# Kernel optimization log

Hardware: AMD Instinct MI355X
Metric: run time of the kernel (lower is better)

Reference implementation:

```python
import jax, jax.numpy as jnp
import numpy as np

D_IN = 2048
D_OUT = 2048
BOUND = 1.0


def setup_inputs() -> dict:
    key = jax.random.key(0)
    kx, kw = jax.random.split(key)
    x = jax.random.normal(kx, (4, 2048, D_IN), dtype=jnp.float32)
    W_raw = 0.02 * jax.random.normal(kw, (D_OUT, D_IN), dtype=jnp.float32)
    return {"x": x, "W_raw": W_raw}


def reference(x, W_raw):
    # sigma = ||W||_2 (largest singular value), exact via SVD
    sigma = jnp.linalg.svd(W_raw, full_matrices=False, compute_uv=False)[0]
    scale = jnp.maximum(sigma / BOUND, 1.0)  # clamp(sigma/bound, min=1)
    Wn = W_raw / scale                        # [d_out, d_in]
    return jnp.einsum('bsi,oi->bso', x, Wn)   # x @ Wn.T
```

## Files before the change

kernel.cpp:

```cpp
#include <hip/hip_runtime.h>
#include <stdint.h>

typedef short bf16x8 __attribute__((ext_vector_type(8)));
typedef float f32x4 __attribute__((ext_vector_type(4)));

__device__ __forceinline__ unsigned short f2bf(float f) {
  union { float f; unsigned int u; } v; v.f = f;
  unsigned int u = v.u;
  return (unsigned short)((u + 0x7FFFu + ((u >> 16) & 1u)) >> 16);
}
__device__ __forceinline__ float bf2f(unsigned short u) {
  union { unsigned int u; float f; } v; v.u = ((unsigned int)u) << 16;
  return v.f;
}
__device__ __forceinline__ void async16(const void* g, void* l) {
  __builtin_amdgcn_global_load_lds(
      (const __attribute__((address_space(1))) unsigned int*)g,
      (__attribute__((address_space(3))) unsigned int*)l, 16, 0, 0);
}

__global__ __launch_bounds__(256) void cast_f32_bf16(
    const float* __restrict__ in, unsigned short* __restrict__ out, int n8) {
  int i = blockIdx.x * 256 + threadIdx.x;
  if (i >= n8) return;
  const float4* p = (const float4*)in;
  float4 a = p[2 * (size_t)i], b = p[2 * (size_t)i + 1];
  union { bf16x8 v; unsigned short s[8]; } o;
  o.s[0] = f2bf(a.x); o.s[1] = f2bf(a.y); o.s[2] = f2bf(a.z); o.s[3] = f2bf(a.w);
  o.s[4] = f2bf(b.x); o.s[5] = f2bf(b.y); o.s[6] = f2bf(b.z); o.s[7] = f2bf(b.w);
  *(bf16x8*)(out + 8 * (size_t)i) = o.v;
}

__device__ __forceinline__ void stage16k(const unsigned short* __restrict__ g0,
                                         int ldK, unsigned short* lds, int tid) {
#pragma unroll
  for (int q = 0; q < 2; ++q) {
    int idx = q * 512 + tid;
    int r = idx >> 3;
    int jj = (idx & 7) ^ (r & 7);
    async16(g0 + (size_t)r * ldK + jj * 8,
            lds + ((size_t)(q * 512 + (tid & ~63))) * 8);
  }
}

template <int OMODE>
__global__ __launch_bounds__(512, 2) void gemm256(
    const unsigned short* __restrict__ A, const unsigned short* __restrict__ B,
    void* __restrict__ Cv, int M, int N, int lda, int K,
    int nTn, int mT, const float* __restrict__ scale_ptr) {
  __shared__ __align__(16) unsigned short AsBuf[3][256 * 64];
  __shared__ __align__(16) unsigned short BsBuf[2][256 * 64];
  const int tid = threadIdx.x;
  const int w = tid >> 6, lane = tid & 63;
  int bid = blockIdx.x;
  const int mb = bid % mT; bid /= mT;
  const int nb = bid % nTn; const int ks = bid / nTn;
  const int m0 = mb * 256, n0 = nb * 256;
  const int wr = w >> 2, wc = w & 3;
  const int R = K >> 7;

  const unsigned short* Ab = A + (size_t)m0 * lda + (size_t)ks * K;
  const unsigned short* Bb = B + (size_t)n0 * lda + (size_t)ks * K;

  unsigned short *a0 = AsBuf[0], *a1 = AsBuf[1], *a2 = AsBuf[2];
  unsigned short *b0 = BsBuf[0], *b1 = BsBuf[1];

  stage16k(Ab,                          lda, a0,            tid);
  stage16k(Ab + (size_t)128 * lda,      lda, a0 + 128 * 64, tid);
  stage16k(Bb,                          lda, b0,            tid);
  stage16k(Bb + (size_t)128 * lda,      lda, b0 + 128 * 64, tid);
  stage16k(Ab + 64,                     lda, a1,            tid);
  stage16k(Ab + 64 + (size_t)128 * lda, lda, a1 + 128 * 64, tid);
  stage16k(Bb + 64,                     lda, b1,            tid);
  stage16k(Bb + 64 + (size_t)128 * lda, lda, b1 + 128 * 64, tid);
  asm volatile("s_waitcnt vmcnt(8)" ::: "memory");
  __builtin_amdgcn_s_barrier();
  asm volatile("" ::: "memory");

  const int fr = lane & 15;
  const int bc0 = ((lane >> 4) << 4) ^ ((fr & 7) << 4);
  const int bc1 = bc0 ^ 64;

  f32x4 acc[8][4] = {};

  for (int r = 0; r < R; ++r) {
    const bool st = (r + 1 < R);
    bf16x8 bg[4][2];
#pragma unroll
    for (int ph = 0; ph < 8; ++ph) {
      const int d = ph >> 2, q = ph & 3;
      const char* cA = (const char*)(d == 0 ? a0 : a1);
      const char* cB = (const char*)(d == 0 ? b0 : b1);
      if (q == 0) {
#pragma unroll
        for (int nf = 0; nf < 4; ++nf) {
          int rb = (wc * 64 + nf * 16 + fr) * 128;
          bg[nf][0] = *(const bf16x8*)(cB + rb + bc0);
          bg[nf][1] = *(const bf16x8*)(cB + rb + bc1);
        }
      }
      bf16x8 af[2][2];
#pragma unroll
      for (int m2 = 0; m2 < 2; ++m2) {
        int rb = (wr * 128 + q * 32 + m2 * 16 + fr) * 128;
        af[m2][0] = *(const bf16x8*)(cA + rb + bc0);
        af[m2][1] = *(const bf16x8*)(cA + rb + bc1);
      }
      if (st) switch (ph) {
        case 0: stage16k(Ab + (size_t)(2 * r + 2) * 64, lda, a2, tid); break;
        case 1: stage16k(Ab + (size_t)(2 * r + 2) * 64 + (size_t)128 * lda, lda,
                         a2 + 128 * 64, tid); break;
        case 2: stage16k(Bb + (size_t)(2 * r + 2) * 64, lda, b0, tid); break;
        case 3: stage16k(Bb + (size_t)(2 * r + 2) * 64 + (size_t)128 * lda, lda,
                         b0 + 128 * 64, tid); break;
        case 4: stage16k(Ab + (size_t)(2 * r + 3) * 64, lda, a0, tid); break;
        case 5: stage16k(Ab + (size_t)(2 * r + 3) * 64 + (size_t)128 * lda, lda,
                         a0 + 128 * 64, tid); break;
        case 6: stage16k(Bb + (size_t)(2 * r + 3) * 64, lda, b1, tid); break;
        case 7: stage16k(Bb + (size_t)(2 * r + 3) * 64 + (size_t)128 * lda, lda,
                         b1 + 128 * 64, tid); break;
      }
      asm volatile("" ::: "memory");
      __builtin_amdgcn_s_barrier();
      asm volatile("" ::: "memory");
      __builtin_amdgcn_s_setprio(1);
#pragma unroll
      for (int m2 = 0; m2 < 2; ++m2)
#pragma unroll
        for (int nf = 0; nf < 4; ++nf)
#pragma unroll
          for (int kh = 0; kh < 2; ++kh)
            acc[q * 2 + m2][nf] = __builtin_amdgcn_mfma_f32_16x16x32_bf16(
                af[m2][kh], bg[nf][kh], acc[q * 2 + m2][nf], 0, 0, 0);
      __builtin_amdgcn_s_setprio(0);
      asm volatile("" ::: "memory");
      if (ph == 3) {
        if (st) asm volatile("s_waitcnt vmcnt(8)" ::: "memory");
        else    asm volatile("s_waitcnt vmcnt(0)" ::: "memory");
      } else if (ph == 7) {
        if (st) asm volatile("s_waitcnt vmcnt(8)" ::: "memory");
      }
      __builtin_amdgcn_s_barrier();
      asm volatile("" ::: "memory");
    }
    unsigned short* t = a2; a2 = a1; a1 = a0; a0 = t;
  }

  float sc = 1.0f;
  if (OMODE == 1) sc = *scale_ptr;
  size_t base = (OMODE == 2) ? (size_t)ks * ((size_t)M * N) : 0;
  const int rr0 = m0 + wr * 128 + ((lane >> 4) << 2);
  const int cc0 = n0 + wc * 64 + fr;
#pragma unroll
  for (int mf = 0; mf < 8; ++mf)
#pragma unroll
    for (int nf = 0; nf < 4; ++nf)
#pragma unroll
      for (int tt = 0; tt < 4; ++tt) {
        size_t idx = base + (size_t)(rr0 + mf * 16 + tt) * N + (cc0 + nf * 16);
        if (OMODE == 2) ((unsigned short*)Cv)[idx] = f2bf(acc[mf][nf][tt]);
        else            ((float*)Cv)[idx] = acc[mf][nf][tt] * sc;
      }
}

__global__ __launch_bounds__(256) void reduce_planes_init(
    const unsigned short* __restrict__ P, unsigned short* __restrict__ out,
    int n8, int np, size_t plane, float* __restrict__ t0,
    float* __restrict__ czero) {
  int i = blockIdx.x * 256 + threadIdx.x;
  if (blockIdx.x < 8) {
    int j = blockIdx.x * 256 + threadIdx.x;
    unsigned int h = (unsigned int)j * 2654435761u;
    h ^= h >> 16; h *= 2246822519u; h ^= h >> 13;
    t0[j] = (float)(h & 0xFFFFu) * (1.0f / 65536.0f) - 0.5f;
    if (j == 0) czero[0] = 0.0f;
  }
  if (i >= n8) return;
  float s[8] = {0.f, 0.f, 0.f, 0.f, 0.f, 0.f, 0.f, 0.f};
  for (int p = 0; p < np; ++p) {
    bf16x8 v = *(const bf16x8*)(P + (size_t)p * plane + (size_t)i * 8);
#pragma unroll
    for (int j = 0; j < 8; ++j) s[j] += bf2f((unsigned short)v[j]);
  }
  union { bf16x8 v; unsigned short u[8]; } o;
#pragma unroll
  for (int j = 0; j < 8; ++j) o.u[j] = f2bf(s[j]);
  *(bf16x8*)(out + (size_t)i * 8) = o.v;
}

__global__ __launch_bounds__(256) void power_step_bf16(
    const unsigned short* __restrict__ Am, const float* __restrict__ tin,
    float* __restrict__ tout, const float* __restrict__ cptr) {
  __shared__ __align__(16) float vs[2048];
  __shared__ float wred[4];
  const int tid = threadIdx.x;
  float4 x0 = ((const float4*)tin)[2 * tid];
  float4 x1 = ((const float4*)tin)[2 * tid + 1];
  float ss = x0.x * x0.x + x0.y * x0.y + x0.z * x0.z + x0.w * x0.w +
             x1.x * x1.x + x1.y * x1.y + x1.z * x1.z + x1.w * x1.w;
#pragma unroll
  for (int o = 32; o > 0; o >>= 1) ss += __shfl_xor(ss, o);
  if ((tid & 63) == 0) wred[tid >> 6] = ss;
  __syncthreads();
  float inv = 1.0f / sqrtf(wred[0] + wred[1] + wred[2] + wred[3]);
  float4* vp = (float4*)vs;
  float4 y0 = {x0.x * inv, x0.y * inv, x0.z * inv, x0.w * inv};
  float4 y1 = {x1.x * inv, x1.y * inv, x1.z * inv, x1.w * inv};
  vp[2 * tid] = y0;
  vp[2 * tid + 1] = y1;
  __syncthreads();
  const int row = blockIdx.x * 8 + (tid >> 5);
  const int sub = tid & 31;
  const bf16x8* Ar = (const bf16x8*)(Am + (size_t)row * 2048);
  float s = 0.f;
#pragma unroll 2
  for (int c = sub; c < 256; c += 32) {
    bf16x8 a = Ar[c];
    float4 v0 = vp[2 * c], v1 = vp[2 * c + 1];
    s += bf2f((unsigned short)a[0]) * v0.x + bf2f((unsigned short)a[1]) * v0.y +
         bf2f((unsigned short)a[2]) * v0.z + bf2f((unsigned short)a[3]) * v0.w +
         bf2f((unsigned short)a[4]) * v1.x + bf2f((unsigned short)a[5]) * v1.y +
         bf2f((unsigned short)a[6]) * v1.z + bf2f((unsigned short)a[7]) * v1.w;
  }
#pragma unroll
  for (int o = 16; o > 0; o >>= 1) s += __shfl_xor(s, o);
  if (sub == 0) tout[row] = s - cptr[0] * vs[row];
}

__global__ __launch_bounds__(256) void finalize_rough(
    const float* __restrict__ tk, float* __restrict__ cout) {
  __shared__ float wred[4];
  const int tid = threadIdx.x;
  float4 x0 = ((const float4*)tk)[2 * tid];
  float4 x1 = ((const float4*)tk)[2 * tid + 1];
  float ss = x0.x * x0.x + x0.y * x0.y + x0.z * x0.z + x0.w * x0.w +
             x1.x * x1.x + x1.y * x1.y + x1.z * x1.z + x1.w * x1.w;
#pragma unroll
  for (int o = 32; o > 0; o >>= 1) ss += __shfl_xor(ss, o);
  if ((tid & 63) == 0) wred[tid >> 6] = ss;
  __syncthreads();
  if (tid == 0)
    cout[0] = 0.49f * sqrtf(wred[0] + wred[1] + wred[2] + wred[3]);
}

__global__ __launch_bounds__(256) void finalize_sigma(
    const float* __restrict__ tk, const float* __restrict__ cptr,
    float* __restrict__ inv_scale) {
  __shared__ float wred[4];
  const int tid = threadIdx.x;
  float4 x0 = ((const float4*)tk)[2 * tid];
  float4 x1 = ((const float4*)tk)[2 * tid + 1];
  float ss = x0.x * x0.x + x0.y * x0.y + x0.z * x0.z + x0.w * x0.w +
             x1.x * x1.x + x1.y * x1.y + x1.z * x1.z + x1.w * x1.w;
#pragma unroll
  for (int o = 32; o > 0; o >>= 1) ss += __shfl_xor(ss, o);
  if ((tid & 63) == 0) wred[tid >> 6] = ss;
  __syncthreads();
  if (tid == 0) {
    float lam = sqrtf(wred[0] + wred[1] + wred[2] + wred[3]) + cptr[0];
    float sigma = sqrtf(lam);
    float scl = fmaxf(sigma, 1.0f);
    inv_scale[0] = 1.0f / scl;
  }
}

extern "C" void kernel_launch(void* const* d_in, const int* in_sizes, int n_in,
                              void* d_out, int out_size, void* d_ws, size_t ws_size,
                              hipStream_t stream) {
  (void)in_sizes; (void)n_in; (void)out_size; (void)ws_size;
  const float* x = (const float*)d_in[0];
  const float* W = (const float*)d_in[1];
  float* out = (float*)d_out;
  char* ws = (char*)d_ws;
  const int K = 2048, N = 2048, M = 4 * 2048;
  const size_t PLANE = (size_t)2048 * 2048;

  unsigned short* xb = (unsigned short*)(ws);
  unsigned short* Wb = (unsigned short*)(ws + ((size_t)32 << 20));
  unsigned short* P1 = (unsigned short*)(ws + ((size_t)40 << 20));
  unsigned short* Am = P1;
  float* tv = (float*)(ws + ((size_t)72 << 20));
  float* inv_scale = tv + 4096;
  float* czero = tv + 4097;
  float* cshift = tv + 4098;

  cast_f32_bf16<<<(M * K / 8 + 255) / 256, 256, 0, stream>>>(x, xb, M * K / 8);
  cast_f32_bf16<<<(N * K / 8 + 255) / 256, 256, 0, stream>>>(W, Wb, N * K / 8);

  gemm256<2><<<256, 512, 0, stream>>>(Wb, Wb, P1, 2048, 2048, 2048, 512, 8, 8, nullptr);
  reduce_planes_init<<<2048, 256, 0, stream>>>(P1, Am, (int)(PLANE / 8), 4, PLANE,
                                               tv, czero);

  int s = 0;
  for (; s < 5; ++s)
    power_step_bf16<<<256, 256, 0, stream>>>(Am, tv + (s & 1) * 2048,
                                             tv + ((s + 1) & 1) * 2048, czero);
  finalize_rough<<<1, 256, 0, stream>>>(tv + (s & 1) * 2048, cshift);
  for (; s < 22; ++s)
    power_step_bf16<<<256, 256, 0, stream>>>(Am, tv + (s & 1) * 2048,
                                             tv + ((s + 1) & 1) * 2048, cshift);
  finalize_sigma<<<1, 256, 0, stream>>>(tv + (s & 1) * 2048, cshift, inv_scale);

  gemm256<1><<<256, 512, 0, stream>>>(xb, Wb, out, M, N, K, K, 8, 32, inv_scale);
}
```

Measured before the change: 198.2 us.

## Fuse x bf16 cast into power-iteration steps and fold rough finalize

The standalone cast of x to bf16 is removed. Its work is split into 22 chunks, and each chunk is done inside one of the 22 latency-bound power_step launches, with the loads issued early and the stores done at the end. The separate finalize_rough kernel is also dropped: a templated MODE 1 power step computes the shift from the input norm itself and writes it out for the later steps. The goal is to hide the cast's bandwidth cost behind small, underutilized kernels and to cut one launch. In exchange, each power step carries extra register pressure and memory traffic.

```diff
diff --git a/kernel.cpp b/kernel.cpp
--- a/kernel.cpp
+++ b/kernel.cpp
@@ -17,6 +17,13 @@
   __builtin_amdgcn_global_load_lds(
       (const __attribute__((address_space(1))) unsigned int*)g,
       (__attribute__((address_space(3))) unsigned int*)l, 16, 0, 0);
+}
+__device__ __forceinline__ void cast8(const float4 a, const float4 b,
+                                      unsigned short* dst) {
+  union { bf16x8 v; unsigned short s[8]; } o;
+  o.s[0] = f2bf(a.x); o.s[1] = f2bf(a.y); o.s[2] = f2bf(a.z); o.s[3] = f2bf(a.w);
+  o.s[4] = f2bf(b.x); o.s[5] = f2bf(b.y); o.s[6] = f2bf(b.z); o.s[7] = f2bf(b.w);
+  *(bf16x8*)dst = o.v;
 }
 
 __global__ __launch_bounds__(256) void cast_f32_bf16(
@@ -24,11 +31,7 @@
   int i = blockIdx.x * 256 + threadIdx.x;
   if (i >= n8) return;
   const float4* p = (const float4*)in;
-  float4 a = p[2 * (size_t)i], b = p[2 * (size_t)i + 1];
-  union { bf16x8 v; unsigned short s[8]; } o;
-  o.s[0] = f2bf(a.x); o.s[1] = f2bf(a.y); o.s[2] = f2bf(a.z); o.s[3] = f2bf(a.w);
-  o.s[4] = f2bf(b.x); o.s[5] = f2bf(b.y); o.s[6] = f2bf(b.z); o.s[7] = f2bf(b.w);
-  *(bf16x8*)(out + 8 * (size_t)i) = o.v;
+  cast8(p[2 * (size_t)i], p[2 * (size_t)i + 1], out + 8 * (size_t)i);
 }
 
 __device__ __forceinline__ void stage16k(const unsigned short* __restrict__ g0,
@@ -188,12 +191,24 @@
   *(bf16x8*)(out + (size_t)i * 8) = o.v;
 }
 
+template <int MODE>
 __global__ __launch_bounds__(256) void power_step_bf16(
     const unsigned short* __restrict__ Am, const float* __restrict__ tin,
-    float* __restrict__ tout, const float* __restrict__ cptr) {
+    float* __restrict__ tout, const float* __restrict__ cptr,
+    float* __restrict__ cwrite, const float* __restrict__ xsrc,
+    unsigned short* __restrict__ xdst, int u0, int u1) {
   __shared__ __align__(16) float vs[2048];
   __shared__ float wred[4];
   const int tid = threadIdx.x;
+
+  const int cu0 = u0 + blockIdx.x * 256 + tid;
+  const int cu1 = cu0 + 65536;
+  const bool cd0 = cu0 < u1, cd1 = cu1 < u1;
+  float4 ca0, cb0, ca1, cb1;
+  const float4* xp = (const float4*)xsrc;
+  if (cd0) { ca0 = xp[2 * (size_t)cu0]; cb0 = xp[2 * (size_t)cu0 + 1]; }
+  if (cd1) { ca1 = xp[2 * (size_t)cu1]; cb1 = xp[2 * (size_t)cu1 + 1]; }
+
   float4 x0 = ((const float4*)tin)[2 * tid];
   float4 x1 = ((const float4*)tin)[2 * tid + 1];
   float ss = x0.x * x0.x + x0.y * x0.y + x0.z * x0.z + x0.w * x0.w +
@@ -202,7 +217,15 @@
   for (int o = 32; o > 0; o >>= 1) ss += __shfl_xor(ss, o);
   if ((tid & 63) == 0) wred[tid >> 6] = ss;
   __syncthreads();
-  float inv = 1.0f / sqrtf(wred[0] + wred[1] + wred[2] + wred[3]);
+  float nrm = sqrtf(wred[0] + wred[1] + wred[2] + wred[3]);
+  float c;
+  if (MODE == 1) {
+    c = 0.49f * nrm;
+    if (blockIdx.x == 0 && tid == 0) cwrite[0] = c;
+  } else {
+    c = cptr[0];
+  }
+  float inv = 1.0f / nrm;
   float4* vp = (float4*)vs;
   float4 y0 = {x0.x * inv, x0.y * inv, x0.z * inv, x0.w * inv};
   float4 y1 = {x1.x * inv, x1.y * inv, x1.z * inv, x1.w * inv};
@@ -214,9 +237,9 @@
   const bf16x8* Ar = (const bf16x8*)(Am + (size_t)row * 2048);
   float s = 0.f;
 #pragma unroll 2
-  for (int c = sub; c < 256; c += 32) {
-    bf16x8 a = Ar[c];
-    float4 v0 = vp[2 * c], v1 = vp[2 * c + 1];
+  for (int cc = sub; cc < 256; cc += 32) {
+    bf16x8 a = Ar[cc];
+    float4 v0 = vp[2 * cc], v1 = vp[2 * cc + 1];
     s += bf2f((unsigned short)a[0]) * v0.x + bf2f((unsigned short)a[1]) * v0.y +
          bf2f((unsigned short)a[2]) * v0.z + bf2f((unsigned short)a[3]) * v0.w +
          bf2f((unsigned short)a[4]) * v1.x + bf2f((unsigned short)a[5]) * v1.y +
@@ -224,23 +247,10 @@
   }
 #pragma unroll
   for (int o = 16; o > 0; o >>= 1) s += __shfl_xor(s, o);
-  if (sub == 0) tout[row] = s - cptr[0] * vs[row];
-}
-
-__global__ __launch_bounds__(256) void finalize_rough(
-    const float* __restrict__ tk, float* __restrict__ cout) {
-  __shared__ float wred[4];
-  const int tid = threadIdx.x;
-  float4 x0 = ((const float4*)tk)[2 * tid];
-  float4 x1 = ((const float4*)tk)[2 * tid + 1];
-  float ss = x0.x * x0.x + x0.y * x0.y + x0.z * x0.z + x0.w * x0.w +
-             x1.x * x1.x + x1.y * x1.y + x1.z * x1.z + x1.w * x1.w;
-#pragma unroll
-  for (int o = 32; o > 0; o >>= 1) ss += __shfl_xor(ss, o);
-  if ((tid & 63) == 0) wred[tid >> 6] = ss;
-  __syncthreads();
-  if (tid == 0)
-    cout[0] = 0.49f * sqrtf(wred[0] + wred[1] + wred[2] + wred[3]);
+  if (sub == 0) tout[row] = s - c * vs[row];
+
+  if (cd0) cast8(ca0, cb0, xdst + 8 * (size_t)cu0);
+  if (cd1) cast8(ca1, cb1, xdst + 8 * (size_t)cu1);
 }
 
 __global__ __launch_bounds__(256) void finalize_sigma(
@@ -284,21 +294,27 @@
   float* czero = tv + 4097;
   float* cshift = tv + 4098;
 
-  cast_f32_bf16<<<(M * K / 8 + 255) / 256, 256, 0, stream>>>(x, xb, M * K / 8);
   cast_f32_bf16<<<(N * K / 8 + 255) / 256, 256, 0, stream>>>(W, Wb, N * K / 8);
 
   gemm256<2><<<256, 512, 0, stream>>>(Wb, Wb, P1, 2048, 2048, 2048, 512, 8, 8, nullptr);
   reduce_planes_init<<<2048, 256, 0, stream>>>(P1, Am, (int)(PLANE / 8), 4, PLANE,
                                                tv, czero);
 
+  const int XU = M * K / 8;
+  const int CH = (XU + 21) / 22;
   int s = 0;
   for (; s < 5; ++s)
-    power_step_bf16<<<256, 256, 0, stream>>>(Am, tv + (s & 1) * 2048,
-                                             tv + ((s + 1) & 1) * 2048, czero);
-  finalize_rough<<<1, 256, 0, stream>>>(tv + (s & 1) * 2048, cshift);
+    power_step_bf16<0><<<256, 256, 0, stream>>>(
+        Am, tv + (s & 1) * 2048, tv + ((s + 1) & 1) * 2048, czero, nullptr,
+        x, xb, s * CH, min((s + 1) * CH, XU));
+  power_step_bf16<1><<<256, 256, 0, stream>>>(
+      Am, tv + (s & 1) * 2048, tv + ((s + 1) & 1) * 2048, czero, cshift,
+      x, xb, s * CH, min((s + 1) * CH, XU));
+  ++s;
   for (; s < 22; ++s)
-    power_step_bf16<<<256, 256, 0, stream>>>(Am, tv + (s & 1) * 2048,
-                                             tv + ((s + 1) & 1) * 2048, cshift);
+    power_step_bf16<0><<<256, 256, 0, stream>>>(
+        Am, tv + (s & 1) * 2048, tv + ((s + 1) & 1) * 2048, cshift, nullptr,
+        x, xb, s * CH, min((s + 1) * CH, XU));
   finalize_sigma<<<1, 256, 0, stream>>>(tv + (s & 1) * 2048, cshift, inv_scale);
 
   gemm256<1><<<256, 512, 0, stream>>>(xb, Wb, out, M, N, K, K, 8, 32, inv_scale);
```

Result: no change. 200.7 us (+1.3%).

## Use Chebyshev-accelerated power iteration and overlap x cast with GEMV steps

Applied to the files above, without the earlier changes.

Replaces the shifted power iteration (22 steps plus a rough-shift kernel) with 3 plain steps, a normalisation step and 13 Chebyshev three-term recurrence steps, then one final step, for 18 GEMV launches in total. The separate x fp32-to-bf16 cast kernel is removed and its work is split into 18 slices, each done inside one of the latency-bound GEMV launches. The GEMV uses 512 threads with one wave per row and preloads the row registers before the reduction. This cuts launch count and hides the x cast behind the GEMV chain, but the accuracy of the sigma estimate now depends on the Chebyshev recurrence and the chosen scaling constants.

```diff
diff --git a/kernel.cpp b/kernel.cpp
--- a/kernel.cpp
+++ b/kernel.cpp
@@ -17,6 +17,19 @@
   __builtin_amdgcn_global_load_lds(
       (const __attribute__((address_space(1))) unsigned int*)g,
       (__attribute__((address_space(3))) unsigned int*)l, 16, 0, 0);
+}
+__device__ __forceinline__ void cast8(const float4 a, const float4 b,
+                                      unsigned short* dst) {
+  union { bf16x8 v; unsigned short s[8]; } o;
+  o.s[0] = f2bf(a.x); o.s[1] = f2bf(a.y); o.s[2] = f2bf(a.z); o.s[3] = f2bf(a.w);
+  o.s[4] = f2bf(b.x); o.s[5] = f2bf(b.y); o.s[6] = f2bf(b.z); o.s[7] = f2bf(b.w);
+  *(bf16x8*)dst = o.v;
+}
+__device__ __forceinline__ float dot8(bf16x8 a, float4 v0, float4 v1) {
+  return bf2f((unsigned short)a[0]) * v0.x + bf2f((unsigned short)a[1]) * v0.y +
+         bf2f((unsigned short)a[2]) * v0.z + bf2f((unsigned short)a[3]) * v0.w +
+         bf2f((unsigned short)a[4]) * v1.x + bf2f((unsigned short)a[5]) * v1.y +
+         bf2f((unsigned short)a[6]) * v1.z + bf2f((unsigned short)a[7]) * v1.w;
 }
 
 __global__ __launch_bounds__(256) void cast_f32_bf16(
@@ -24,11 +37,7 @@
   int i = blockIdx.x * 256 + threadIdx.x;
   if (i >= n8) return;
   const float4* p = (const float4*)in;
-  float4 a = p[2 * (size_t)i], b = p[2 * (size_t)i + 1];
-  union { bf16x8 v; unsigned short s[8]; } o;
-  o.s[0] = f2bf(a.x); o.s[1] = f2bf(a.y); o.s[2] = f2bf(a.z); o.s[3] = f2bf(a.w);
-  o.s[4] = f2bf(b.x); o.s[5] = f2bf(b.y); o.s[6] = f2bf(b.z); o.s[7] = f2bf(b.w);
-  *(bf16x8*)(out + 8 * (size_t)i) = o.v;
+  cast8(p[2 * (size_t)i], p[2 * (size_t)i + 1], out + 8 * (size_t)i);
 }
 
 __device__ __forceinline__ void stage16k(const unsigned short* __restrict__ g0,
@@ -188,59 +197,69 @@
   *(bf16x8*)(out + (size_t)i * 8) = o.v;
 }
 
-__global__ __launch_bounds__(256) void power_step_bf16(
+template <int MODE>
+__global__ __launch_bounds__(512) void gemv_step(
     const unsigned short* __restrict__ Am, const float* __restrict__ tin,
-    float* __restrict__ tout, const float* __restrict__ cptr) {
+    float* __restrict__ tout, float* __restrict__ ch, float* __restrict__ aux,
+    const float* __restrict__ xsrc, unsigned short* __restrict__ xdst,
+    int u0, int u1) {
   __shared__ __align__(16) float vs[2048];
-  __shared__ float wred[4];
+  __shared__ float wred[8];
   const int tid = threadIdx.x;
-  float4 x0 = ((const float4*)tin)[2 * tid];
-  float4 x1 = ((const float4*)tin)[2 * tid + 1];
-  float ss = x0.x * x0.x + x0.y * x0.y + x0.z * x0.z + x0.w * x0.w +
-             x1.x * x1.x + x1.y * x1.y + x1.z * x1.z + x1.w * x1.w;
-#pragma unroll
-  for (int o = 32; o > 0; o >>= 1) ss += __shfl_xor(ss, o);
-  if ((tid & 63) == 0) wred[tid >> 6] = ss;
+  const int wv = tid >> 6, lane = tid & 63;
+  const int row = blockIdx.x * 8 + wv;
+
+  const bf16x8* Ar = (const bf16x8*)(Am + (size_t)row * 2048);
+  bf16x8 ar0 = Ar[lane], ar1 = Ar[lane + 64];
+  bf16x8 ar2 = Ar[lane + 128], ar3 = Ar[lane + 192];
+  const int cu = u0 + blockIdx.x * 512 + tid;
+  const bool cd = cu < u1;
+  float4 ca, cb;
+  if (cd) {
+    ca = ((const float4*)xsrc)[2 * (size_t)cu];
+    cb = ((const float4*)xsrc)[2 * (size_t)cu + 1];
+  }
+  float ymv = 0.f, chv = 0.f;
+  if (MODE == 3) { ymv = aux[row]; chv = ch[0]; }
+
+  float4 x0 = ((const float4*)tin)[tid];
+  float sin_ = 1.0f;
+  if (MODE != 3) {
+    float ss = x0.x * x0.x + x0.y * x0.y + x0.z * x0.z + x0.w * x0.w;
+#pragma unroll
+    for (int o = 32; o > 0; o >>= 1) ss += __shfl_xor(ss, o);
+    if (lane == 0) wred[wv] = ss;
+    __syncthreads();
+    float n2 = 0.f;
+#pragma unroll
+    for (int j = 0; j < 8; ++j) n2 += wred[j];
+    float nrm = sqrtf(n2);
+    if (MODE == 2) {
+      chv = nrm;
+      if (blockIdx.x == 0 && tid == 0) ch[0] = nrm;
+    }
+    sin_ = 1.0f / nrm;
+  }
+  float4 y = {x0.x * sin_, x0.y * sin_, x0.z * sin_, x0.w * sin_};
+  ((float4*)vs)[tid] = y;
   __syncthreads();
-  float inv = 1.0f / sqrtf(wred[0] + wred[1] + wred[2] + wred[3]);
-  float4* vp = (float4*)vs;
-  float4 y0 = {x0.x * inv, x0.y * inv, x0.z * inv, x0.w * inv};
-  float4 y1 = {x1.x * inv, x1.y * inv, x1.z * inv, x1.w * inv};
-  vp[2 * tid] = y0;
-  vp[2 * tid + 1] = y1;
-  __syncthreads();
-  const int row = blockIdx.x * 8 + (tid >> 5);
-  const int sub = tid & 31;
-  const bf16x8* Ar = (const bf16x8*)(Am + (size_t)row * 2048);
-  float s = 0.f;
-#pragma unroll 2
-  for (int c = sub; c < 256; c += 32) {
-    bf16x8 a = Ar[c];
-    float4 v0 = vp[2 * c], v1 = vp[2 * c + 1];
-    s += bf2f((unsigned short)a[0]) * v0.x + bf2f((unsigned short)a[1]) * v0.y +
-         bf2f((unsigned short)a[2]) * v0.z + bf2f((unsigned short)a[3]) * v0.w +
-         bf2f((unsigned short)a[4]) * v1.x + bf2f((unsigned short)a[5]) * v1.y +
-         bf2f((unsigned short)a[6]) * v1.z + bf2f((unsigned short)a[7]) * v1.w;
-  }
-#pragma unroll
-  for (int o = 16; o > 0; o >>= 1) s += __shfl_xor(s, o);
-  if (sub == 0) tout[row] = s - cptr[0] * vs[row];
-}
-
-__global__ __launch_bounds__(256) void finalize_rough(
-    const float* __restrict__ tk, float* __restrict__ cout) {
-  __shared__ float wred[4];
-  const int tid = threadIdx.x;
-  float4 x0 = ((const float4*)tk)[2 * tid];
-  float4 x1 = ((const float4*)tk)[2 * tid + 1];
-  float ss = x0.x * x0.x + x0.y * x0.y + x0.z * x0.z + x0.w * x0.w +
-             x1.x * x1.x + x1.y * x1.y + x1.z * x1.z + x1.w * x1.w;
-#pragma unroll
-  for (int o = 32; o > 0; o >>= 1) ss += __shfl_xor(ss, o);
-  if ((tid & 63) == 0) wred[tid >> 6] = ss;
-  __syncthreads();
-  if (tid == 0)
-    cout[0] = 0.49f * sqrtf(wred[0] + wred[1] + wred[2] + wred[3]);
+
+  const float4* vp = (const float4*)vs;
+  float s = dot8(ar0, vp[2 * lane], vp[2 * lane + 1]);
+  s += dot8(ar1, vp[2 * (lane + 64)], vp[2 * (lane + 64) + 1]);
+  s += dot8(ar2, vp[2 * (lane + 128)], vp[2 * (lane + 128) + 1]);
+  s += dot8(ar3, vp[2 * (lane + 192)], vp[2 * (lane + 192) + 1]);
+#pragma unroll
+  for (int o = 32; o > 0; o >>= 1) s += __shfl_xor(s, o);
+  if (lane == 0) {
+    float r;
+    if (MODE == 0)      r = s;
+    else if (MODE == 2) r = (2.0f / chv) * s - vs[row];
+    else                r = (4.0f / chv) * s - 2.0f * vs[row] - ymv;
+    tout[row] = r;
+    if (MODE == 2) aux[row] = vs[row];
+  }
+  if (cd) cast8(ca, cb, xdst + 8 * (size_t)cu);
 }
 
 __global__ __launch_bounds__(256) void finalize_sigma(
@@ -280,26 +299,37 @@
   unsigned short* P1 = (unsigned short*)(ws + ((size_t)40 << 20));
   unsigned short* Am = P1;
   float* tv = (float*)(ws + ((size_t)72 << 20));
-  float* inv_scale = tv + 4096;
-  float* czero = tv + 4097;
-  float* cshift = tv + 4098;
-
-  cast_f32_bf16<<<(M * K / 8 + 255) / 256, 256, 0, stream>>>(x, xb, M * K / 8);
+  float* tb0 = tv, *tb1 = tv + 2048, *tb2 = tv + 4096;
+  float* inv_scale = tv + 6144;
+  float* czero = tv + 6145;
+  float* cshift = tv + 6146;
+  float* tb[3] = {tb0, tb1, tb2};
+
   cast_f32_bf16<<<(N * K / 8 + 255) / 256, 256, 0, stream>>>(W, Wb, N * K / 8);
 
   gemm256<2><<<256, 512, 0, stream>>>(Wb, Wb, P1, 2048, 2048, 2048, 512, 8, 8, nullptr);
   reduce_planes_init<<<2048, 256, 0, stream>>>(P1, Am, (int)(PLANE / 8), 4, PLANE,
-                                               tv, czero);
-
-  int s = 0;
-  for (; s < 5; ++s)
-    power_step_bf16<<<256, 256, 0, stream>>>(Am, tv + (s & 1) * 2048,
-                                             tv + ((s + 1) & 1) * 2048, czero);
-  finalize_rough<<<1, 256, 0, stream>>>(tv + (s & 1) * 2048, cshift);
-  for (; s < 22; ++s)
-    power_step_bf16<<<256, 256, 0, stream>>>(Am, tv + (s & 1) * 2048,
-                                             tv + ((s + 1) & 1) * 2048, cshift);
-  finalize_sigma<<<1, 256, 0, stream>>>(tv + (s & 1) * 2048, cshift, inv_scale);
+                                               tb0, czero);
+
+  const int XU = M * K / 8;
+  const int NL = 18;
+  const int CH = (XU + NL - 1) / NL;
+  int li = 0;
+#define SLICE x, xb, (li) * CH, min((li + 1) * CH, XU)); ++li
+  gemv_step<0><<<256, 512, 0, stream>>>(Am, tb0, tb1, cshift, czero, SLICE;
+  gemv_step<0><<<256, 512, 0, stream>>>(Am, tb1, tb0, cshift, czero, SLICE;
+  gemv_step<0><<<256, 512, 0, stream>>>(Am, tb0, tb1, cshift, czero, SLICE;
+  gemv_step<2><<<256, 512, 0, stream>>>(Am, tb1, tb2, cshift, tb0, SLICE;
+  int cy = 2, cm = 0;
+  for (int k = 0; k < 13; ++k) {
+    int co = 3 - cy - cm;
+    gemv_step<3><<<256, 512, 0, stream>>>(Am, tb[cy], tb[co], cshift, tb[cm], SLICE;
+    cm = cy; cy = co;
+  }
+  int co = 3 - cy - cm;
+  gemv_step<0><<<256, 512, 0, stream>>>(Am, tb[cy], tb[co], cshift, czero, SLICE;
+#undef SLICE
+  finalize_sigma<<<1, 256, 0, stream>>>(tb[co], czero, inv_scale);
 
   gemm256<1><<<256, 512, 0, stream>>>(xb, Wb, out, M, N, K, K, 8, 32, inv_scale);
 }
```

Measured after the change: 172.6 us. 12.9% less time.
